# Kernel optimization log

Hardware: AMD Instinct MI355X
Metric: run time of the kernel (lower is better)

Reference implementation:

```python
import jax, jax.numpy as jnp
import numpy as np

B, T, D, H = 8, 1024, 512, 8
CH = D // H          # chunk_size = d_model // num_heads
PAD = 0              # pad_token_id
MAX_TRANS = 1024     # translen cap from source
NINF = float('-inf')


def setup_inputs() -> dict:
    key = jax.random.key(0)
    ks = jax.random.split(key, 8)
    features = jax.random.normal(ks[0], (B, T, D), jnp.float32)
    pos_embed = jax.random.normal(ks[1], (B, T, D), jnp.float32)
    tokens = jax.random.randint(ks[2], (B, T), 0, 32000, dtype=jnp.int32)
    Wq = jax.random.normal(ks[3], (D, 2 * D), jnp.float32) * 0.02
    bq = jnp.zeros((D,), jnp.float32)
    Wk = jax.random.normal(ks[4], (D, 2 * D), jnp.float32) * 0.02
    bk = jnp.zeros((D,), jnp.float32)
    Wg = jax.random.normal(ks[5], (H, 2 * D), jnp.float32) * 0.02
    bg = jnp.zeros((H,), jnp.float32)
    return dict(features=features, pos_embed=pos_embed, tokens=tokens,
                Wq=Wq, bq=bq, Wk=Wk, bk=bk, Wg=Wg, bg=bg)


def _safe_log_softmax(x, axis):
    # matches torch F.log_softmax followed by re-masking: rows that are all -inf stay -inf
    m = jnp.max(x, axis=axis, keepdims=True)
    allinf = jnp.isneginf(m)
    m_safe = jnp.where(allinf, 0.0, m)
    lse = m_safe + jnp.log(jnp.sum(jnp.exp(x - m_safe), axis=axis, keepdims=True))
    lse = jnp.where(allinf, 0.0, lse)
    return x - lse


def _safe_logsumexp(x, axis):
    # matches the custom logsumexp helper in the source (all -inf -> -inf, no nan)
    m = jnp.max(x, axis=axis)
    mask = jnp.isneginf(m)
    m_safe = jnp.where(mask, 0.0, m)
    s = jnp.sum(jnp.exp(x - jnp.expand_dims(m_safe, axis)), axis=axis)
    return jnp.log(jnp.where(mask, 1.0, s)) + jnp.where(mask, NINF, m_safe)


def reference(features, pos_embed, tokens, Wq, bq, Wk, bk, Wg, bg):
    # features_withpos = cat(decoder_out, link positional embedding)  -> [B, T, 2D]
    f = jnp.concatenate([features, pos_embed], axis=-1)
    q = (f @ Wq.T + bq).reshape(B, T, H, CH)
    k = (f @ Wk.T + bk).reshape(B, T, H, CH)
    log_gates = jax.nn.log_softmax(f @ Wg.T + bg, axis=-1)  # [B, T, H]
    # einsum 'bicf,bjcf->bijc' with c = head chunk
    scores = jnp.einsum('bihc,bjhc->bijh', q, k) / np.float32(np.sqrt(CH))  # [B,T,T,H]

    translen = min(MAX_TRANS, T - 1)
    n_valid = jnp.sum(tokens != PAD, axis=-1)  # [B]
    # banded indices: position i links to positions i+1 .. i+translen
    band_idx = jnp.arange(T)[:, None] + jnp.arange(translen)[None, :] + 1  # [T, translen]
    invalid = band_idx[None, :, :] >= n_valid[:, None, None]               # [B, T, translen]
    idx_c = jnp.where(invalid, 0, band_idx[None, :, :])
    idx_full = jnp.broadcast_to(idx_c[..., None], (B, T, translen, H))
    extract = jnp.take_along_axis(scores, idx_full, axis=2)                # [B,T,translen,H]
    extract = jnp.where(invalid[..., None], NINF, extract)
    # normalize over transition axis, then mask fully-invalid rows back to -inf
    extract = _safe_log_softmax(extract, axis=2)
    nouse = jnp.all(invalid, axis=-1)                                      # [B, T]
    extract = jnp.where(nouse[:, :, None, None], NINF, extract)
    # head-gated logsumexp over heads -> banded links [B, T, translen]
    links_band = _safe_logsumexp(extract + log_gates[:, :, None, :], axis=-1)
    # restore_valid_links: scatter band back to full [B, T, T] (-inf elsewhere)
    rel = jnp.arange(T)[None, :] - jnp.arange(T)[:, None] - 1              # [T, T]
    valid = (rel >= 0) & (rel < translen)
    rel_c = jnp.clip(rel, 0, translen - 1)
    rel_full = jnp.broadcast_to(rel_c[None, :, :], (B, T, T))
    out = jnp.take_along_axis(links_band, rel_full, axis=2)
    return jnp.where(valid[None, :, :], out, NINF)
```

## Files before the change

### kernel.cpp

```cpp
#include <hip/hip_runtime.h>
#include <math.h>

#define BATCH 8
#define T 1024
#define NH 8
#define NROW 8192
#define NEG_INF (-INFINITY)
#define SENT (-1.0e30f)

typedef __attribute__((ext_vector_type(8))) short short8;
typedef __attribute__((ext_vector_type(4))) float f32x4;

__device__ __forceinline__ ushort f2bf(float x) {
  uint u = __float_as_uint(x);
  return (ushort)((u + 0x7FFFu + ((u >> 16) & 1u)) >> 16);
}
__device__ __forceinline__ uint pack2(float a, float b) {
  return (uint)f2bf(a) | ((uint)f2bf(b) << 16);
}
__device__ __forceinline__ void gl_lds16(const ushort* g, ushort* l) {
  __builtin_amdgcn_global_load_lds(
      (const __attribute__((address_space(1))) unsigned int*)g,
      (__attribute__((address_space(3))) unsigned int*)l, 16, 0, 0);
}

__global__ __launch_bounds__(256) void k_nvalid(const int* __restrict__ tokens,
                                                int* __restrict__ nv) {
  int b = blockIdx.x, t = threadIdx.x;
  int cnt = 0;
  for (int i = t; i < T; i += 256) cnt += (tokens[b * T + i] != 0) ? 1 : 0;
  __shared__ int s[256];
  s[t] = cnt;
  __syncthreads();
  for (int st = 128; st > 0; st >>= 1) {
    if (t < st) s[t] += s[t + st];
    __syncthreads();
  }
  if (t == 0) nv[b] = s[0];
}

__global__ __launch_bounds__(256) void k_prep_w(const float* __restrict__ Wq,
                                                const float* __restrict__ Wk,
                                                ushort* __restrict__ Wbf) {
  const int gid = blockIdx.x * 256 + threadIdx.x;
  const int e0 = gid * 8;
  const int n = e0 >> 10, k = e0 & 1023;
  const float* src = (n < 512) ? (Wq + (size_t)n * 1024 + k)
                               : (Wk + (size_t)(n - 512) * 1024 + k);
  float4 a = *(const float4*)src;
  float4 b = *(const float4*)(src + 4);
  uint4 o;
  o.x = pack2(a.x, a.y); o.y = pack2(a.z, a.w);
  o.z = pack2(b.x, b.y); o.w = pack2(b.z, b.w);
  *(uint4*)(Wbf + (size_t)n * 1024 + k) = o;
}

__global__ __launch_bounds__(256) void k_prep_fg(
    const float* __restrict__ feat, const float* __restrict__ pos,
    const float* __restrict__ Wg, const float* __restrict__ bg,
    ushort* __restrict__ fbf, float* __restrict__ gout) {
  __shared__ __align__(16) float Ws[8192];
  const int tid = threadIdx.x;
#pragma unroll
  for (int u = 0; u < 8; ++u)
    ((float4*)Ws)[u * 256 + tid] = ((const float4*)Wg)[u * 256 + tid];
  __syncthreads();

  const int w = tid >> 6, l = tid & 63;
  const int c0 = l * 16;
  const int row0 = blockIdx.x * 8 + w * 2;

  float4 f[2][4];
#pragma unroll
  for (int r = 0; r < 2; ++r) {
    const int row = row0 + r;
    const float* src = (c0 < 512) ? (feat + (size_t)row * 512 + c0)
                                  : (pos + (size_t)row * 512 + (c0 - 512));
#pragma unroll
    for (int q4 = 0; q4 < 4; ++q4) f[r][q4] = *(const float4*)(src + q4 * 4);
    uint4 o0, o1;
    o0.x = pack2(f[r][0].x, f[r][0].y); o0.y = pack2(f[r][0].z, f[r][0].w);
    o0.z = pack2(f[r][1].x, f[r][1].y); o0.w = pack2(f[r][1].z, f[r][1].w);
    o1.x = pack2(f[r][2].x, f[r][2].y); o1.y = pack2(f[r][2].z, f[r][2].w);
    o1.z = pack2(f[r][3].x, f[r][3].y); o1.w = pack2(f[r][3].z, f[r][3].w);
    *(uint4*)(fbf + (size_t)row * 1024 + c0) = o0;
    *(uint4*)(fbf + (size_t)row * 1024 + c0 + 8) = o1;
  }

  float s[2][8];
#pragma unroll
  for (int h = 0; h < 8; ++h) {
    const float* wg = Ws + h * 1024 + c0;
    float4 w0 = *(const float4*)(wg + 0);
    float4 w1 = *(const float4*)(wg + 4);
    float4 w2 = *(const float4*)(wg + 8);
    float4 w3 = *(const float4*)(wg + 12);
#pragma unroll
    for (int r = 0; r < 2; ++r)
      s[r][h] = f[r][0].x * w0.x + f[r][0].y * w0.y + f[r][0].z * w0.z + f[r][0].w * w0.w
              + f[r][1].x * w1.x + f[r][1].y * w1.y + f[r][1].z * w1.z + f[r][1].w * w1.w
              + f[r][2].x * w2.x + f[r][2].y * w2.y + f[r][2].z * w2.z + f[r][2].w * w2.w
              + f[r][3].x * w3.x + f[r][3].y * w3.y + f[r][3].z * w3.z + f[r][3].w * w3.w;
  }
#pragma unroll
  for (int m = 1; m < 64; m <<= 1)
#pragma unroll
    for (int r = 0; r < 2; ++r)
#pragma unroll
      for (int h = 0; h < 8; ++h) s[r][h] += __shfl_xor(s[r][h], m, 64);
  if (l == 0) {
#pragma unroll
    for (int r = 0; r < 2; ++r) {
      float lg[8], mx = -1e30f;
#pragma unroll
      for (int h = 0; h < 8; ++h) { lg[h] = s[r][h] + bg[h]; mx = fmaxf(mx, lg[h]); }
      float sum = 0.f;
#pragma unroll
      for (int h = 0; h < 8; ++h) sum += __expf(lg[h] - mx);
      const float lse = mx + __logf(sum);
#pragma unroll
      for (int h = 0; h < 8; ++h) gout[(size_t)(row0 + r) * 8 + h] = lg[h] - lse;
    }
  }
}

__global__ __launch_bounds__(256) void k_gemm(
    const ushort* __restrict__ fbf, const ushort* __restrict__ Wbf,
    const float* __restrict__ bq, const float* __restrict__ bk,
    ushort* __restrict__ qbuf, ushort* __restrict__ kbuf) {
  const int g = blockIdx.x + 8 * blockIdx.y;
  const int wid = (g & 7) * 64 + (g >> 3);
  const int n0 = (wid & 7) * 128;
  const int m0 = (wid >> 3) * 128;
  const int tid = threadIdx.x;
  const int w = tid >> 6, l = tid & 63;
  const int lo = l & 15, quad = l >> 4;
  const int wm0 = (w >> 1) * 64, wn0 = (w & 1) * 64;

  __shared__ ushort As[128 * 64];
  __shared__ ushort Bs[128 * 64];

  f32x4 acc[4][4];
#pragma unroll
  for (int i = 0; i < 4; ++i)
#pragma unroll
    for (int j = 0; j < 4; ++j) acc[i][j] = (f32x4){0.f, 0.f, 0.f, 0.f};

  const int c8 = (tid & 7) * 8;
  const int r0 = tid >> 3;
  ushort* lA = As + (size_t)w * 512;
  ushort* lB = Bs + (size_t)w * 512;

  for (int k0 = 0; k0 < 1024; k0 += 64) {
    __syncthreads();
#pragma unroll
    for (int u = 0; u < 4; ++u) {
      gl_lds16(fbf + (size_t)(m0 + u * 32 + r0) * 1024 + k0 + c8, lA + u * 2048);
      gl_lds16(Wbf + (size_t)(n0 + u * 32 + r0) * 1024 + k0 + c8, lB + u * 2048);
    }
    __syncthreads();
#pragma unroll
    for (int kk = 0; kk < 2; ++kk) {
      short8 af[4], bfr[4];
#pragma unroll
      for (int mi = 0; mi < 4; ++mi)
        af[mi] = *(const short8*)(As + (size_t)(wm0 + mi * 16 + lo) * 64 + kk * 32 + quad * 8);
#pragma unroll
      for (int ni = 0; ni < 4; ++ni)
        bfr[ni] = *(const short8*)(Bs + (size_t)(wn0 + ni * 16 + lo) * 64 + kk * 32 + quad * 8);
#pragma unroll
      for (int mi = 0; mi < 4; ++mi)
#pragma unroll
        for (int ni = 0; ni < 4; ++ni)
          acc[mi][ni] = __builtin_amdgcn_mfma_f32_16x16x32_bf16(af[mi], bfr[ni], acc[mi][ni], 0, 0, 0);
    }
  }

  float bv[4];
#pragma unroll
  for (int ni = 0; ni < 4; ++ni) {
    const int gn = n0 + wn0 + ni * 16 + lo;
    bv[ni] = (gn < 512) ? bq[gn] : bk[gn - 512];
  }
#pragma unroll
  for (int mi = 0; mi < 4; ++mi)
#pragma unroll
    for (int ni = 0; ni < 4; ++ni) {
      const int gn = n0 + wn0 + ni * 16 + lo;
      ushort* dst = (gn < 512) ? (qbuf + gn) : (kbuf + gn - 512);
#pragma unroll
      for (int r = 0; r < 4; ++r) {
        const int m = m0 + wm0 + mi * 16 + quad * 4 + r;
        dst[(size_t)m * 512] = f2bf(acc[mi][ni][r] + bv[ni]);
      }
    }
}

__global__ __launch_bounds__(256) void k_pass1(
    const ushort* __restrict__ q, const ushort* __restrict__ kv,
    const float* __restrict__ g, const int* __restrict__ nvp,
    float* __restrict__ Wt) {
  const int it = blockIdx.x, h = blockIdx.y, b = blockIdx.z;
  const int nv = nvp[b];
  const int i0 = it * 64;
  const int tid = threadIdx.x;
  const int w = tid >> 6, l = tid & 63;
  const int lo = l & 15, quad = l >> 4;

  __shared__ ushort Ks[2][64 * 64];

  const ushort* qp = q + (size_t)(b * T + i0 + w * 16 + lo) * 512 + h * 64 + quad * 8;
  const short8 a0 = *(const short8*)qp;
  const short8 a1 = *(const short8*)(qp + 32);

  float lsum[4] = {0.f, 0.f, 0.f, 0.f};
  const int ntile = ((nv + 63) >> 6) - it;

  if (ntile > 0) {
    auto stage = [&](int buf, int jt) {
#pragma unroll
      for (int u = 0; u < 2; ++u) {
        const int s = u * 256 + tid;
        const int row = s >> 3, c = s & 7;
        gl_lds16(kv + (size_t)(b * T + jt * 64 + row) * 512 + h * 64 + ((c ^ (row & 7)) * 8),
                 Ks[buf] + (size_t)(u * 256 + w * 64) * 8);
      }
    };
    stage(0, it);
    __syncthreads();
    for (int s = 0; s < ntile; ++s) {
      if (s + 1 < ntile) stage((s + 1) & 1, it + s + 1);
      const ushort* kbase = Ks[s & 1];
      const int j0 = (it + s) * 64;
#pragma unroll
      for (int ni = 0; ni < 4; ++ni) {
        const int rw = ni * 16 + lo;
        const short8 b0 = *(const short8*)(kbase + (size_t)rw * 64 + ((quad ^ (rw & 7)) * 8));
        const short8 b1 = *(const short8*)(kbase + (size_t)rw * 64 + (((4 + quad) ^ (rw & 7)) * 8));
        f32x4 acc = (f32x4){0.f, 0.f, 0.f, 0.f};
        acc = __builtin_amdgcn_mfma_f32_16x16x32_bf16(a0, b0, acc, 0, 0, 0);
        acc = __builtin_amdgcn_mfma_f32_16x16x32_bf16(a1, b1, acc, 0, 0, 0);
        const int j = j0 + ni * 16 + lo;
#pragma unroll
        for (int r = 0; r < 4; ++r) {
          const int i = i0 + w * 16 + quad * 4 + r;
          if (j > i && j < nv) lsum[r] += __expf(acc[r] * 0.125f);
        }
      }
      __syncthreads();
    }
  }

#pragma unroll
  for (int m = 1; m < 16; m <<= 1)
#pragma unroll
    for (int r = 0; r < 4; ++r) lsum[r] += __shfl_xor(lsum[r], m, 64);
  if (lo == 0) {
#pragma unroll
    for (int r = 0; r < 4; ++r) {
      const size_t row = (size_t)(b * T) + i0 + w * 16 + quad * 4 + r;
      Wt[(size_t)h * NROW + row] =
          (lsum[r] > 0.f) ? (g[row * 8 + h] - __logf(lsum[r])) : NEG_INF;
    }
  }
}

__global__ __launch_bounds__(256) void k_pass2(
    const ushort* __restrict__ q, const ushort* __restrict__ kv,
    const float* __restrict__ Wt, const int* __restrict__ nvp,
    float* __restrict__ out) {
  const int jt = blockIdx.x, it = blockIdx.y, b = blockIdx.z;
  const int nv = nvp[b];
  const int i0 = it * 64, j0 = jt * 64;
  const int tid = threadIdx.x;

  if (jt < it || j0 >= nv) {
    const int r0 = tid >> 4, c0 = (tid & 15) * 4;
    float4 v; v.x = v.y = v.z = v.w = SENT;
#pragma unroll
    for (int u = 0; u < 4; ++u)
      *(float4*)(out + ((size_t)(b * T + i0 + r0 + u * 16)) * T + j0 + c0) = v;
    return;
  }

  const int w = tid >> 6, l = tid & 63;
  const int lo = l & 15, quad = l >> 4;
  const int irow = i0 + w * 16 + quad * 4;

  __shared__ ushort Ks[64 * 512];

#pragma unroll
  for (int u = 0; u < 16; ++u) {
    const int row = u * 4 + w;
    gl_lds16(kv + (size_t)(b * T + j0 + row) * 512 + ((l ^ (row & 7)) * 8),
             Ks + (size_t)(u * 256 + w * 64) * 8);
  }

  const ushort* qb = q + (size_t)(b * T + i0 + w * 16 + lo) * 512 + quad * 8;
  short8 qa0[8], qa1[8];
#pragma unroll
  for (int h = 0; h < 8; ++h) {
    qa0[h] = *(const short8*)(qb + h * 64);
    qa1[h] = *(const short8*)(qb + h * 64 + 32);
  }

  float se[4][4];
#pragma unroll
  for (int a = 0; a < 4; ++a)
#pragma unroll
    for (int c = 0; c < 4; ++c) se[a][c] = 0.f;

  __syncthreads();

#pragma unroll
  for (int h = 0; h < 8; ++h) {
    const float4 wv = *(const float4*)(Wt + (size_t)h * NROW + b * T + irow);
#pragma unroll
    for (int ni = 0; ni < 4; ++ni) {
      const int rw = ni * 16 + lo;
      const int cs0 = (h * 8 + quad) ^ (rw & 7);
      const int cs1 = (h * 8 + 4 + quad) ^ (rw & 7);
      const short8 b0 = *(const short8*)(Ks + (size_t)rw * 512 + cs0 * 8);
      const short8 b1 = *(const short8*)(Ks + (size_t)rw * 512 + cs1 * 8);
      f32x4 acc = (f32x4){0.f, 0.f, 0.f, 0.f};
      acc = __builtin_amdgcn_mfma_f32_16x16x32_bf16(qa0[h], b0, acc, 0, 0, 0);
      acc = __builtin_amdgcn_mfma_f32_16x16x32_bf16(qa1[h], b1, acc, 0, 0, 0);
      se[ni][0] += __expf(acc[0] * 0.125f + wv.x);
      se[ni][1] += __expf(acc[1] * 0.125f + wv.y);
      se[ni][2] += __expf(acc[2] * 0.125f + wv.z);
      se[ni][3] += __expf(acc[3] * 0.125f + wv.w);
    }
  }

#pragma unroll
  for (int ni = 0; ni < 4; ++ni) {
    const int j = j0 + ni * 16 + lo;
#pragma unroll
    for (int r = 0; r < 4; ++r) {
      const int i = irow + r;
      out[((size_t)(b * T + i)) * T + j] =
          (j > i && j < nv) ? fmaxf(__logf(se[ni][r]), SENT) : SENT;
    }
  }
}

extern "C" void kernel_launch(void* const* d_in, const int* in_sizes, int n_in,
                              void* d_out, int out_size, void* d_ws, size_t ws_size,
                              hipStream_t stream) {
  (void)in_sizes; (void)n_in; (void)out_size; (void)ws_size;
  const float* feat = (const float*)d_in[0];
  const float* pos  = (const float*)d_in[1];
  const int* tokens = (const int*)d_in[2];
  const float* Wq = (const float*)d_in[3];
  const float* bq = (const float*)d_in[4];
  const float* Wk = (const float*)d_in[5];
  const float* bk = (const float*)d_in[6];
  const float* Wg = (const float*)d_in[7];
  const float* bg = (const float*)d_in[8];
  float* out = (float*)d_out;

  ushort* qbuf = (ushort*)d_ws;
  ushort* kbuf = qbuf + (size_t)NROW * 512;
  ushort* Wbf  = kbuf + (size_t)NROW * 512;
  float*  gbuf = (float*)(Wbf + (size_t)1024 * 1024);
  float*  Wt   = gbuf + (size_t)NROW * NH;
  int*    nv   = (int*)(Wt + (size_t)NH * NROW);

  ushort* fbf = (ushort*)d_out;

  k_nvalid<<<dim3(BATCH), dim3(256), 0, stream>>>(tokens, nv);
  k_prep_w<<<dim3(512), dim3(256), 0, stream>>>(Wq, Wk, Wbf);
  k_prep_fg<<<dim3(1024), dim3(256), 0, stream>>>(feat, pos, Wg, bg, fbf, gbuf);
  k_gemm<<<dim3(8, 64), dim3(256), 0, stream>>>(fbf, Wbf, bq, bk, qbuf, kbuf);
  k_pass1<<<dim3(16, NH, BATCH), dim3(256), 0, stream>>>(qbuf, kbuf, gbuf, nv, Wt);
  k_pass2<<<dim3(16, 16, BATCH), dim3(256), 0, stream>>>(qbuf, kbuf, Wt, nv, out);
}
```

Baseline: 196.4 us.

## Swap MFMA operands for row-contiguous outputs, vectorize stores, use exp2 and skip masked tiles

```diff
diff --git a/kernel.cpp b/kernel.cpp
--- a/kernel.cpp
+++ b/kernel.cpp
@@ -7,6 +7,8 @@
 #define NROW 8192
 #define NEG_INF (-INFINITY)
 #define SENT (-1.0e30f)
+#define SC 0.180336880f
+#define LOG2E 1.442695041f
 
 typedef __attribute__((ext_vector_type(8))) short short8;
 typedef __attribute__((ext_vector_type(4))) float f32x4;
@@ -172,28 +174,32 @@
       for (int mi = 0; mi < 4; ++mi)
 #pragma unroll
         for (int ni = 0; ni < 4; ++ni)
-          acc[mi][ni] = __builtin_amdgcn_mfma_f32_16x16x32_bf16(af[mi], bfr[ni], acc[mi][ni], 0, 0, 0);
-    }
-  }
-
-  float bv[4];
+          acc[mi][ni] = __builtin_amdgcn_mfma_f32_16x16x32_bf16(bfr[ni], af[mi], acc[mi][ni], 0, 0, 0);
+    }
+  }
+
+  float4 bias4[4];
 #pragma unroll
   for (int ni = 0; ni < 4; ++ni) {
-    const int gn = n0 + wn0 + ni * 16 + lo;
-    bv[ni] = (gn < 512) ? bq[gn] : bk[gn - 512];
-  }
-#pragma unroll
-  for (int mi = 0; mi < 4; ++mi)
+    const int gn = n0 + wn0 + ni * 16 + quad * 4;
+    bias4[ni] = *(const float4*)((gn < 512) ? (bq + gn) : (bk + gn - 512));
+  }
+#pragma unroll
+  for (int mi = 0; mi < 4; ++mi) {
+    const int m = m0 + wm0 + mi * 16 + lo;
 #pragma unroll
     for (int ni = 0; ni < 4; ++ni) {
-      const int gn = n0 + wn0 + ni * 16 + lo;
-      ushort* dst = (gn < 512) ? (qbuf + gn) : (kbuf + gn - 512);
-#pragma unroll
-      for (int r = 0; r < 4; ++r) {
-        const int m = m0 + wm0 + mi * 16 + quad * 4 + r;
-        dst[(size_t)m * 512] = f2bf(acc[mi][ni][r] + bv[ni]);
-      }
-    }
+      const int gn = n0 + wn0 + ni * 16 + quad * 4;
+      ushort* dst = (gn < 512) ? (qbuf + (size_t)m * 512 + gn)
+                               : (kbuf + (size_t)m * 512 + gn - 512);
+      ushort4 o;
+      o.x = f2bf(acc[mi][ni][0] + bias4[ni].x);
+      o.y = f2bf(acc[mi][ni][1] + bias4[ni].y);
+      o.z = f2bf(acc[mi][ni][2] + bias4[ni].z);
+      o.w = f2bf(acc[mi][ni][3] + bias4[ni].w);
+      *(ushort4*)dst = o;
+    }
+  }
 }
 
 __global__ __launch_bounds__(256) void k_pass1(
@@ -209,11 +215,12 @@
 
   __shared__ ushort Ks[2][64 * 64];
 
-  const ushort* qp = q + (size_t)(b * T + i0 + w * 16 + lo) * 512 + h * 64 + quad * 8;
+  const int i = i0 + w * 16 + lo;
+  const ushort* qp = q + (size_t)(b * T + i) * 512 + h * 64 + quad * 8;
   const short8 a0 = *(const short8*)qp;
   const short8 a1 = *(const short8*)(qp + 32);
 
-  float lsum[4] = {0.f, 0.f, 0.f, 0.f};
+  float lsum = 0.f;
   const int ntile = ((nv + 63) >> 6) - it;
 
   if (ntile > 0) {
@@ -232,36 +239,39 @@
       if (s + 1 < ntile) stage((s + 1) & 1, it + s + 1);
       const ushort* kbase = Ks[s & 1];
       const int j0 = (it + s) * 64;
+      const bool diag = (s == 0);
+      const bool masked = diag | (j0 + 64 > nv);
 #pragma unroll
       for (int ni = 0; ni < 4; ++ni) {
+        if (diag && ni < w) continue;
         const int rw = ni * 16 + lo;
         const short8 b0 = *(const short8*)(kbase + (size_t)rw * 64 + ((quad ^ (rw & 7)) * 8));
         const short8 b1 = *(const short8*)(kbase + (size_t)rw * 64 + (((4 + quad) ^ (rw & 7)) * 8));
         f32x4 acc = (f32x4){0.f, 0.f, 0.f, 0.f};
-        acc = __builtin_amdgcn_mfma_f32_16x16x32_bf16(a0, b0, acc, 0, 0, 0);
-        acc = __builtin_amdgcn_mfma_f32_16x16x32_bf16(a1, b1, acc, 0, 0, 0);
-        const int j = j0 + ni * 16 + lo;
-#pragma unroll
-        for (int r = 0; r < 4; ++r) {
-          const int i = i0 + w * 16 + quad * 4 + r;
-          if (j > i && j < nv) lsum[r] += __expf(acc[r] * 0.125f);
+        acc = __builtin_amdgcn_mfma_f32_16x16x32_bf16(b0, a0, acc, 0, 0, 0);
+        acc = __builtin_amdgcn_mfma_f32_16x16x32_bf16(b1, a1, acc, 0, 0, 0);
+        if (!masked) {
+#pragma unroll
+          for (int r = 0; r < 4; ++r) lsum += __builtin_amdgcn_exp2f(acc[r] * SC);
+        } else {
+          const int jb = j0 + ni * 16 + quad * 4;
+#pragma unroll
+          for (int r = 0; r < 4; ++r) {
+            const int j = jb + r;
+            if (j > i && j < nv) lsum += __builtin_amdgcn_exp2f(acc[r] * SC);
+          }
         }
       }
       __syncthreads();
     }
   }
 
-#pragma unroll
-  for (int m = 1; m < 16; m <<= 1)
-#pragma unroll
-    for (int r = 0; r < 4; ++r) lsum[r] += __shfl_xor(lsum[r], m, 64);
-  if (lo == 0) {
-#pragma unroll
-    for (int r = 0; r < 4; ++r) {
-      const size_t row = (size_t)(b * T) + i0 + w * 16 + quad * 4 + r;
-      Wt[(size_t)h * NROW + row] =
-          (lsum[r] > 0.f) ? (g[row * 8 + h] - __logf(lsum[r])) : NEG_INF;
-    }
+  lsum += __shfl_xor(lsum, 16, 64);
+  lsum += __shfl_xor(lsum, 32, 64);
+  if (quad == 0) {
+    const size_t row = (size_t)(b * T) + i;
+    Wt[(size_t)h * NROW + row] =
+        (lsum > 0.f) ? (g[row * 8 + h] - __logf(lsum)) : NEG_INF;
   }
 }
 
@@ -285,7 +295,7 @@
 
   const int w = tid >> 6, l = tid & 63;
   const int lo = l & 15, quad = l >> 4;
-  const int irow = i0 + w * 16 + quad * 4;
+  const int i = i0 + w * 16 + lo;
 
   __shared__ ushort Ks[64 * 512];
 
@@ -296,12 +306,14 @@
              Ks + (size_t)(u * 256 + w * 64) * 8);
   }
 
-  const ushort* qb = q + (size_t)(b * T + i0 + w * 16 + lo) * 512 + quad * 8;
+  const ushort* qb = q + (size_t)(b * T + i) * 512 + quad * 8;
   short8 qa0[8], qa1[8];
+  float wl[8];
 #pragma unroll
   for (int h = 0; h < 8; ++h) {
     qa0[h] = *(const short8*)(qb + h * 64);
     qa1[h] = *(const short8*)(qb + h * 64 + 32);
+    wl[h] = Wt[(size_t)h * NROW + b * T + i] * LOG2E;
   }
 
   float se[4][4];
@@ -314,7 +326,6 @@
 
 #pragma unroll
   for (int h = 0; h < 8; ++h) {
-    const float4 wv = *(const float4*)(Wt + (size_t)h * NROW + b * T + irow);
 #pragma unroll
     for (int ni = 0; ni < 4; ++ni) {
       const int rw = ni * 16 + lo;
@@ -323,24 +334,24 @@
       const short8 b0 = *(const short8*)(Ks + (size_t)rw * 512 + cs0 * 8);
       const short8 b1 = *(const short8*)(Ks + (size_t)rw * 512 + cs1 * 8);
       f32x4 acc = (f32x4){0.f, 0.f, 0.f, 0.f};
-      acc = __builtin_amdgcn_mfma_f32_16x16x32_bf16(qa0[h], b0, acc, 0, 0, 0);
-      acc = __builtin_amdgcn_mfma_f32_16x16x32_bf16(qa1[h], b1, acc, 0, 0, 0);
-      se[ni][0] += __expf(acc[0] * 0.125f + wv.x);
-      se[ni][1] += __expf(acc[1] * 0.125f + wv.y);
-      se[ni][2] += __expf(acc[2] * 0.125f + wv.z);
-      se[ni][3] += __expf(acc[3] * 0.125f + wv.w);
-    }
-  }
-
+      acc = __builtin_amdgcn_mfma_f32_16x16x32_bf16(b0, qa0[h], acc, 0, 0, 0);
+      acc = __builtin_amdgcn_mfma_f32_16x16x32_bf16(b1, qa1[h], acc, 0, 0, 0);
+#pragma unroll
+      for (int r = 0; r < 4; ++r)
+        se[ni][r] += __builtin_amdgcn_exp2f(acc[r] * SC + wl[h]);
+    }
+  }
+
+  const size_t orow = ((size_t)(b * T + i)) * T;
 #pragma unroll
   for (int ni = 0; ni < 4; ++ni) {
-    const int j = j0 + ni * 16 + lo;
-#pragma unroll
-    for (int r = 0; r < 4; ++r) {
-      const int i = irow + r;
-      out[((size_t)(b * T + i)) * T + j] =
-          (j > i && j < nv) ? fmaxf(__logf(se[ni][r]), SENT) : SENT;
-    }
+    const int jb = j0 + ni * 16 + quad * 4;
+    float4 v;
+    v.x = (jb + 0 > i && jb + 0 < nv) ? fmaxf(__logf(se[ni][0]), SENT) : SENT;
+    v.y = (jb + 1 > i && jb + 1 < nv) ? fmaxf(__logf(se[ni][1]), SENT) : SENT;
+    v.z = (jb + 2 > i && jb + 2 < nv) ? fmaxf(__logf(se[ni][2]), SENT) : SENT;
+    v.w = (jb + 3 > i && jb + 3 < nv) ? fmaxf(__logf(se[ni][3]), SENT) : SENT;
+    *(float4*)(out + orow + jb) = v;
   }
 }
 
```

Result: faster. 189.8 us (-3.4%).
